# Kernel tuning notes

Measured on AMD Instinct MI355X. Metric: run time of the kernel, lower is better.

The kernel has to match this reference:

```python
import jax, jax.numpy as jnp
import numpy as np

BSZ, SEQ, EMBED = 2, 4096, 1024
NUM_HEADS = 16
HEAD_DIM = EMBED // NUM_HEADS
WINDOW = 256  # attention_window[layer_id]


def setup_inputs() -> dict:
    key = jax.random.key(0)
    ks = jax.random.split(key, 7)
    s = 1.0 / np.sqrt(EMBED)
    return {
        "hidden_states": jax.random.normal(ks[0], (BSZ, SEQ, EMBED), jnp.float32),
        "Wq": jax.random.normal(ks[1], (EMBED, EMBED), jnp.float32) * s,
        "bq": jnp.zeros((EMBED,), jnp.float32),
        "Wk": jax.random.normal(ks[2], (EMBED, EMBED), jnp.float32) * s,
        "bk": jnp.zeros((EMBED,), jnp.float32),
        "Wv": jax.random.normal(ks[3], (EMBED, EMBED), jnp.float32) * s,
        "bv": jnp.zeros((EMBED,), jnp.float32),
    }


def _blocks3(x, nb, w):
    # x: [b, s + 2w, h, d] -> [b, nb, 3w, h, d]; block c sees key blocks c-1, c, c+1
    b = x.shape[0]
    xb = x.reshape(b, nb + 2, w, NUM_HEADS, HEAD_DIM)
    return jnp.concatenate([xb[:, i:i + nb] for i in range(3)], axis=2)


def reference(hidden_states, Wq, bq, Wk, bk, Wv, bv):
    b, s, e = hidden_states.shape
    w = WINDOW
    nb = s // w
    q = (hidden_states @ Wq + bq) * (1.0 / np.sqrt(HEAD_DIM))
    k = hidden_states @ Wk + bk
    v = hidden_states @ Wv + bv
    q = q.reshape(b, nb, w, NUM_HEADS, HEAD_DIM)
    k = k.reshape(b, s, NUM_HEADS, HEAD_DIM)
    v = v.reshape(b, s, NUM_HEADS, HEAD_DIM)
    pad = ((0, 0), (w, w), (0, 0), (0, 0))
    kb = _blocks3(jnp.pad(k, pad), nb, w)  # [b, nb, 3w, h, d]
    vb = _blocks3(jnp.pad(v, pad), nb, w)
    # banded scores: query x in block n attends keys at global pos n*w - w + y
    scores = jnp.einsum('bnxhd,bnyhd->bnhxy', q, kb)  # [b, nb, h, w, 3w]
    x_idx = jnp.arange(w)
    y_idx = jnp.arange(3 * w)
    band = jnp.abs(y_idx[None, :] - x_idx[:, None] - w) <= w  # [w, 3w]
    kpos = jnp.arange(nb)[:, None] * w - w + y_idx[None, :]   # [nb, 3w]
    inb = (kpos >= 0) & (kpos < s)
    mask = band[None, :, :] & inb[:, None, :]                 # [nb, w, 3w]
    scores = jnp.where(mask[None, :, None, :, :], scores, -jnp.inf)
    probs = jax.nn.softmax(scores.astype(jnp.float32), axis=-1).astype(v.dtype)
    attn = jnp.einsum('bnhxy,bnyhd->bnxhd', probs, vb)        # [b, nb, w, h, d]
    return attn.reshape(b, s, e)
```

## Files before the change

kernel.cpp:

```cpp
#include <hip/hip_runtime.h>
#include <stdint.h>

#define SEQ    4096
#define EMBED  1024
#define NHEAD  16
#define HDIM   64
#define WIN    256
#define BSZ    2
#define M_TOT  (BSZ * SEQ)
#define N_QKV  3072
#define N_QK   2048
#define K_DIM  1024
#define LOG2E  1.4426950408889634f

typedef __attribute__((ext_vector_type(8))) __bf16 bf16x8;
typedef __attribute__((ext_vector_type(4))) float  f32x4;

__device__ __forceinline__ unsigned short f2bf(float f) {
  union { float f; unsigned int u; } c; c.f = f;
  unsigned int u = c.u;
  unsigned int r = (u + 0x7FFFu + ((u >> 16) & 1u)) >> 16;
  return (unsigned short)r;
}

__device__ __forceinline__ unsigned int cvt_pk_bf16(float lo, float hi) {
  unsigned int r;
  asm("v_cvt_pk_bf16_f32 %0, %1, %2" : "=v"(r) : "v"(lo), "v"(hi));
  return r;
}

__device__ __forceinline__ void gl2lds16(const void* g, void* l) {
  __builtin_amdgcn_global_load_lds((const __attribute__((address_space(1))) void*)g,
                                   (__attribute__((address_space(3))) void*)l, 16, 0, 0);
}

__global__ __launch_bounds__(256) void cvt_all(const float* __restrict__ in,
                                               unsigned short* __restrict__ out,
                                               const float* __restrict__ Wq,
                                               const float* __restrict__ Wk,
                                               const float* __restrict__ Wv,
                                               unsigned short* __restrict__ Wt) {
  __shared__ float t[32][33];
  int tid = threadIdx.x;
  if (blockIdx.x < 8192) {
    int i = (blockIdx.x * 256 + tid) * 4;
    float4 v = *(const float4*)(in + i);
    ushort4 o;
    o.x = f2bf(v.x); o.y = f2bf(v.y); o.z = f2bf(v.z); o.w = f2bf(v.w);
    *(ushort4*)(out + i) = o;
  } else {
    int wb = blockIdx.x - 8192;
    int z  = wb >> 10;
    int rem = wb & 1023;
    int kb = (rem & 31) * 32, nb = (rem >> 5) * 32;
    const float* W = (z == 0) ? Wq : (z == 1) ? Wk : Wv;
    int tx = tid & 31, ty = tid >> 5;
    for (int it = 0; it < 4; ++it) {
      int k = kb + ty + it * 8;
      t[ty + it * 8][tx] = W[(size_t)k * 1024 + nb + tx];
    }
    __syncthreads();
    for (int it = 0; it < 4; ++it) {
      int n = nb + ty + it * 8;
      Wt[(size_t)(z * 1024 + n) * 1024 + kb + tx] = f2bf(t[tx][ty + it * 8]);
    }
  }
}

__global__ __launch_bounds__(512, 2) void qkv_gemm(const unsigned short* __restrict__ A,
                                                   const unsigned short* __restrict__ Bt,
                                                   const float* __restrict__ bq,
                                                   const float* __restrict__ bk,
                                                   const float* __restrict__ bv,
                                                   unsigned short* __restrict__ C,
                                                   unsigned short* __restrict__ Vt) {
  __shared__ unsigned short As[2][128 * 64];
  __shared__ unsigned short Bs[2][384 * 64];
  int tid  = threadIdx.x;
  int lane = tid & 63, wave = tid >> 6;
  int ln   = lane & 15, quad = lane >> 4;
  int flat = blockIdx.y * 8 + blockIdx.x;
  int swz  = (flat & 7) * 64 + (flat >> 3);
  int m0 = (swz >> 3) * 128, n0 = (swz & 7) * 384;
  int wy = wave >> 2, wx = wave & 3;
  f32x4 acc[4][6];
#pragma unroll
  for (int i = 0; i < 4; ++i)
#pragma unroll
    for (int j = 0; j < 6; ++j) acc[i][j] = (f32x4){0.f, 0.f, 0.f, 0.f};

  int c8 = tid & 7;

#define STG_A(buf, kt)                                                           \
  do {                                                                           \
    _Pragma("unroll")                                                            \
    for (int s = 0; s < 2; ++s) {                                                \
      int r = s * 64 + (tid >> 3); int cg = c8 ^ (r & 7);                        \
      gl2lds16(A + (size_t)(m0 + r) * K_DIM + (size_t)(kt) * 64 + cg * 8,        \
               &As[buf][r * 64 + c8 * 8]);                                       \
    }                                                                            \
  } while (0)
#define STG_B(buf, jreg, kt)                                                     \
  do {                                                                           \
    _Pragma("unroll")                                                            \
    for (int s = 0; s < 2; ++s) {                                                \
      int r = s * 64 + (tid >> 3); int gr = (jreg) * 128 + r;                    \
      int cg = c8 ^ (gr & 7);                                                    \
      gl2lds16(Bt + (size_t)(n0 + gr) * K_DIM + (size_t)(kt) * 64 + cg * 8,      \
               &Bs[buf][gr * 64 + c8 * 8]);                                      \
    }                                                                            \
  } while (0)

  STG_A(0, 0); STG_B(0, 0, 0); STG_B(0, 1, 0); STG_B(0, 2, 0);
  STG_B(1, 0, 1); STG_B(1, 1, 1); STG_B(1, 2, 1);
  asm volatile("s_waitcnt vmcnt(6)" ::: "memory");
  __builtin_amdgcn_s_barrier();

  int aBase = wy * 64, bBase = wx * 96;

#pragma unroll 1
  for (int t = 0; t < 16; ++t) {
    int cur = t & 1;
    const unsigned short* as = As[cur];
    const unsigned short* bs = Bs[cur];
    bf16x8 af[4][2], bf01[2][2], bf23[2][2], bf45[2][2];

#pragma unroll
    for (int i2 = 0; i2 < 4; ++i2) {
      int row = aBase + i2 * 16 + ln;
#pragma unroll
      for (int ks = 0; ks < 2; ++ks) {
        int c = (ks * 4 + quad) ^ (row & 7);
        af[i2][ks] = *(const bf16x8*)&as[row * 64 + c * 8];
      }
    }
#pragma unroll
    for (int j2 = 0; j2 < 2; ++j2) {
      int row = bBase + j2 * 16 + ln;
#pragma unroll
      for (int ks = 0; ks < 2; ++ks) {
        int c = (ks * 4 + quad) ^ (row & 7);
        bf01[j2][ks] = *(const bf16x8*)&bs[row * 64 + c * 8];
      }
    }
    if (t < 15) STG_A(cur ^ 1, t + 1);
    __builtin_amdgcn_s_barrier();
    __builtin_amdgcn_s_setprio(1);
#pragma unroll
    for (int ks = 0; ks < 2; ++ks)
#pragma unroll
      for (int i2 = 0; i2 < 4; ++i2)
#pragma unroll
        for (int j2 = 0; j2 < 2; ++j2)
          acc[i2][j2] = __builtin_amdgcn_mfma_f32_16x16x32_bf16(af[i2][ks], bf01[j2][ks], acc[i2][j2], 0, 0, 0);
    __builtin_amdgcn_s_setprio(0);
    __builtin_amdgcn_s_barrier();

#pragma unroll
    for (int j2 = 0; j2 < 2; ++j2) {
      int row = bBase + 32 + j2 * 16 + ln;
#pragma unroll
      for (int ks = 0; ks < 2; ++ks) {
        int c = (ks * 4 + quad) ^ (row & 7);
        bf23[j2][ks] = *(const bf16x8*)&bs[row * 64 + c * 8];
      }
    }
    __builtin_amdgcn_s_barrier();
    __builtin_amdgcn_s_setprio(1);
#pragma unroll
    for (int ks = 0; ks < 2; ++ks)
#pragma unroll
      for (int i2 = 0; i2 < 4; ++i2)
#pragma unroll
        for (int j2 = 0; j2 < 2; ++j2)
          acc[i2][2 + j2] = __builtin_amdgcn_mfma_f32_16x16x32_bf16(af[i2][ks], bf23[j2][ks], acc[i2][2 + j2], 0, 0, 0);
    __builtin_amdgcn_s_setprio(0);
    __builtin_amdgcn_s_barrier();

#pragma unroll
    for (int j2 = 0; j2 < 2; ++j2) {
      int row = bBase + 64 + j2 * 16 + ln;
#pragma unroll
      for (int ks = 0; ks < 2; ++ks) {
        int c = (ks * 4 + quad) ^ (row & 7);
        bf45[j2][ks] = *(const bf16x8*)&bs[row * 64 + c * 8];
      }
    }
    __builtin_amdgcn_s_barrier();
    __builtin_amdgcn_s_setprio(1);
#pragma unroll
    for (int ks = 0; ks < 2; ++ks)
#pragma unroll
      for (int i2 = 0; i2 < 4; ++i2)
        acc[i2][4] = __builtin_amdgcn_mfma_f32_16x16x32_bf16(af[i2][ks], bf45[0][ks], acc[i2][4], 0, 0, 0);
    __builtin_amdgcn_s_setprio(0);
    if (t < 14) STG_B(cur, 0, t + 2);
    __builtin_amdgcn_s_barrier();

    if (t < 14) { STG_B(cur, 1, t + 2); STG_B(cur, 2, t + 2); }
    __builtin_amdgcn_s_barrier();
    __builtin_amdgcn_s_setprio(1);
#pragma unroll
    for (int ks = 0; ks < 2; ++ks)
#pragma unroll
      for (int i2 = 0; i2 < 4; ++i2)
        acc[i2][5] = __builtin_amdgcn_mfma_f32_16x16x32_bf16(af[i2][ks], bf45[1][ks], acc[i2][5], 0, 0, 0);
    __builtin_amdgcn_s_setprio(0);
    if (t < 14) asm volatile("s_waitcnt vmcnt(6)" ::: "memory");
    else        asm volatile("s_waitcnt vmcnt(0)" ::: "memory");
    __builtin_amdgcn_s_barrier();
  }
#undef STG_A
#undef STG_B

#pragma unroll
  for (int j = 0; j < 6; ++j) {
    int n = n0 + wx * 96 + j * 16 + ln;
    if (n < N_QK) {
      float bias, scl;
      if (n < 1024) { bias = bq[n];        scl = 0.125f * LOG2E; }
      else          { bias = bk[n - 1024]; scl = 1.f; }
#pragma unroll
      for (int i = 0; i < 4; ++i) {
        int mb = m0 + wy * 64 + i * 16 + quad * 4;
#pragma unroll
        for (int r = 0; r < 4; ++r) {
          float v = (acc[i][j][r] + bias) * scl;
          C[(size_t)(mb + r) * N_QK + n] = f2bf(v);
        }
      }
    } else {
      int hd = n - 2048;
      float bias = bv[hd];
#pragma unroll
      for (int i = 0; i < 4; ++i) {
        int mb  = m0 + wy * 64 + i * 16 + quad * 4;
        int bb  = mb >> 12;
        int pos = mb & (SEQ - 1);
        ushort4 pk;
        pk.x = f2bf(acc[i][j][0] + bias);
        pk.y = f2bf(acc[i][j][1] + bias);
        pk.z = f2bf(acc[i][j][2] + bias);
        pk.w = f2bf(acc[i][j][3] + bias);
        *(ushort4*)&Vt[((size_t)bb * (NHEAD * HDIM) + hd) * SEQ + pos] = pk;
      }
    }
  }
}

__global__ __launch_bounds__(256) void attn(const unsigned short* __restrict__ qk,
                                            const unsigned short* __restrict__ vtg,
                                            float* __restrict__ out) {
  __shared__ unsigned short Kl[64 * 72];
  __shared__ unsigned short Vl[64 * 72];
  int tid  = threadIdx.x;
  int lane = tid & 63, wave = tid >> 6;
  int ln   = lane & 15, quad = lane >> 4;
  int bx = blockIdx.x;
  int lx = ((bx & 7) << 3) | (bx >> 3);
  int q0 = lx * 64, head = blockIdx.y, b = blockIdx.z;
  size_t baseRow = (size_t)b * SEQ;
  const unsigned short* kptr = qk + 1024;
  const unsigned short* vrow = vtg + ((size_t)(b * NHEAD + head) * HDIM) * SEQ;

  int sy = tid >> 3, sc = tid & 7;
  const unsigned short* kbase = kptr + (baseRow + sy) * (size_t)N_QK + head * HDIM + sc * 8;
  const unsigned short* vbase = vrow + (size_t)sy * SEQ + sc * 8;

  bf16x8 qf[2];
  {
    size_t ro = (baseRow + q0 + wave * 16 + ln) * (size_t)N_QK + head * HDIM + quad * 8;
    qf[0] = *(const bf16x8*)&qk[ro];
    qf[1] = *(const bf16x8*)&qk[ro + 32];
  }

  float l_st = 0.f;
  f32x4 o_acc[4];
  for (int dt = 0; dt < 4; ++dt) o_acc[dt] = (f32x4){0.f, 0.f, 0.f, 0.f};

  int lo = (q0 >= 256) ? 0 : (256 - q0) / 64;
  int hi = (SEQ + 256 - q0) / 64; if (hi > 9) hi = 9;

  uint4 pkA0, pkA1, pvA0, pvA1;
  uint4 pkB0, pkB1, pvB0, pvB1;
#define PREFETCH_A(KT)                                                      \
  {                                                                         \
    pkA0 = *(const uint4*)&kbase[(size_t)(KT) * N_QK];                      \
    pkA1 = *(const uint4*)&kbase[(size_t)((KT) + 32) * N_QK];               \
    pvA0 = *(const uint4*)&vbase[(KT)];                                     \
    pvA1 = *(const uint4*)&vbase[(size_t)32 * SEQ + (KT)];                  \
  }
#define PREFETCH_B(KT)                                                      \
  {                                                                         \
    pkB0 = *(const uint4*)&kbase[(size_t)(KT) * N_QK];                      \
    pkB1 = *(const uint4*)&kbase[(size_t)((KT) + 32) * N_QK];               \
    pvB0 = *(const uint4*)&vbase[(KT)];                                     \
    pvB1 = *(const uint4*)&vbase[(size_t)32 * SEQ + (KT)];                  \
  }

  PREFETCH_A(q0 - 256 + lo * 64);
  if (lo + 1 < hi) PREFETCH_B(q0 - 256 + (lo + 1) * 64);

  int srcA = ((lane & 16) << 1) | ln;
  int srcB = srcA + 16;
  bool hiQ = (lane & 32) != 0;

  for (int t = lo; t < hi; ++t) {
    int kt = q0 - 256 + t * 64;
    bool useA = ((t - lo) & 1) == 0;

    asm volatile("s_waitcnt lgkmcnt(0)" ::: "memory");
    __builtin_amdgcn_sched_barrier(0);
    __builtin_amdgcn_s_barrier();
    if (useA) {
      *(uint4*)&Kl[sy * 72 + sc * 8]        = pkA0;
      *(uint4*)&Kl[(sy + 32) * 72 + sc * 8] = pkA1;
      *(uint4*)&Vl[sy * 72 + sc * 8]        = pvA0;
      *(uint4*)&Vl[(sy + 32) * 72 + sc * 8] = pvA1;
    } else {
      *(uint4*)&Kl[sy * 72 + sc * 8]        = pkB0;
      *(uint4*)&Kl[(sy + 32) * 72 + sc * 8] = pkB1;
      *(uint4*)&Vl[sy * 72 + sc * 8]        = pvB0;
      *(uint4*)&Vl[(sy + 32) * 72 + sc * 8] = pvB1;
    }
    asm volatile("s_waitcnt lgkmcnt(0)" ::: "memory");
    __builtin_amdgcn_sched_barrier(0);
    __builtin_amdgcn_s_barrier();

    if (t + 2 < hi) {
      if (useA) PREFETCH_A(kt + 128) else PREFETCH_B(kt + 128)
    }

    f32x4 s[4];
    __builtin_amdgcn_s_setprio(1);
    for (int nt = 0; nt < 4; ++nt) {
      bf16x8 kf0 = *(const bf16x8*)&Kl[(nt * 16 + ln) * 72 + quad * 8];
      bf16x8 kf1 = *(const bf16x8*)&Kl[(nt * 16 + ln) * 72 + 32 + quad * 8];
      f32x4 z = (f32x4){0.f, 0.f, 0.f, 0.f};
      z = __builtin_amdgcn_mfma_f32_16x16x32_bf16(kf0, qf[0], z, 0, 0, 0);
      z = __builtin_amdgcn_mfma_f32_16x16x32_bf16(kf1, qf[1], z, 0, 0, 0);
      s[nt] = z;
    }
    __builtin_amdgcn_s_setprio(0);

    if (t == 0 || t == 8) {
      int qq = q0 + wave * 16 + ln;
      for (int nt = 0; nt < 4; ++nt) {
        int kb = kt + nt * 16 + quad * 4 - qq;
        for (int r = 0; r < 4; ++r) {
          int dd = kb + r;
          if (dd < -WIN || dd > WIN) s[nt][r] = -INFINITY;
        }
      }
    }

    float rs = 0.f;
    for (int nt = 0; nt < 4; ++nt)
      for (int r = 0; r < 4; ++r) {
        float p = exp2f(s[nt][r]);
        s[nt][r] = p;
        rs += p;
      }
    l_st += rs;

    unsigned int p01[4], p23[4];
    for (int nt = 0; nt < 4; ++nt) {
      p01[nt] = cvt_pk_bf16(s[nt][0], s[nt][1]);
      p23[nt] = cvt_pk_bf16(s[nt][2], s[nt][3]);
    }

    for (int ks = 0; ks < 2; ++ks) {
      int ntA = 2 * ks, ntB = 2 * ks + 1;
      unsigned int a0 = (unsigned int)__shfl((int)p01[ntA], srcA);
      unsigned int a1 = (unsigned int)__shfl((int)p23[ntA], srcA);
      unsigned int a2 = (unsigned int)__shfl((int)p01[ntA], srcB);
      unsigned int a3 = (unsigned int)__shfl((int)p23[ntA], srcB);
      unsigned int b0 = (unsigned int)__shfl((int)p01[ntB], srcA);
      unsigned int b1 = (unsigned int)__shfl((int)p23[ntB], srcA);
      unsigned int b2 = (unsigned int)__shfl((int)p01[ntB], srcB);
      unsigned int b3 = (unsigned int)__shfl((int)p23[ntB], srcB);
      union { uint4 u; bf16x8 v; } pf;
      pf.u.x = hiQ ? b0 : a0;
      pf.u.y = hiQ ? b1 : a1;
      pf.u.z = hiQ ? b2 : a2;
      pf.u.w = hiQ ? b3 : a3;
      __builtin_amdgcn_s_setprio(1);
      for (int dt = 0; dt < 4; ++dt) {
        bf16x8 vf = *(const bf16x8*)&Vl[(dt * 16 + ln) * 72 + ks * 32 + quad * 8];
        o_acc[dt] = __builtin_amdgcn_mfma_f32_16x16x32_bf16(vf, pf.v, o_acc[dt], 0, 0, 0);
      }
      __builtin_amdgcn_s_setprio(0);
    }
  }

  float l = l_st;
  l += __shfl_xor(l, 16);
  l += __shfl_xor(l, 32);
  float inv = 1.0f / l;
  int qpos = q0 + wave * 16 + ln;
  float* ob = out + (baseRow + qpos) * (size_t)EMBED + head * HDIM + quad * 4;
  for (int dt = 0; dt < 4; ++dt) {
    float4 v;
    v.x = o_acc[dt][0] * inv;
    v.y = o_acc[dt][1] * inv;
    v.z = o_acc[dt][2] * inv;
    v.w = o_acc[dt][3] * inv;
    *(float4*)(ob + dt * 16) = v;
  }
#undef PREFETCH_A
#undef PREFETCH_B
}

extern "C" void kernel_launch(void* const* d_in, const int* in_sizes, int n_in,
                              void* d_out, int out_size, void* d_ws, size_t ws_size,
                              hipStream_t stream) {
  const float* h  = (const float*)d_in[0];
  const float* Wq = (const float*)d_in[1];
  const float* bq = (const float*)d_in[2];
  const float* Wk = (const float*)d_in[3];
  const float* bk = (const float*)d_in[4];
  const float* Wv = (const float*)d_in[5];
  const float* bv = (const float*)d_in[6];
  float* out = (float*)d_out;

  unsigned short* h_bf  = (unsigned short*)d_ws;
  unsigned short* wt_bf = h_bf + (size_t)M_TOT * K_DIM;
  unsigned short* qk    = wt_bf + (size_t)N_QKV * K_DIM;
  unsigned short* vtg   = qk + (size_t)M_TOT * N_QK;

  cvt_all<<<8192 + 3072, 256, 0, stream>>>(h, h_bf, Wq, Wk, Wv, wt_bf);
  qkv_gemm<<<dim3(8, 64), 512, 0, stream>>>(h_bf, wt_bf, bq, bk, bv, qk, vtg);
  attn<<<dim3(SEQ / 64, NHEAD, BSZ), 256, 0, stream>>>(qk, vtg, out);
}
```

Before: 214.5 us.

## Merge GEMM tail MFMA phases and reduce attention prefetch to single buffer

In the QKV GEMM, the B-tile global loads for step t+2 are now issued together before one merged MFMA phase, which drops two barriers per k-step. In the attention kernel, the two-deep register double-buffered K/V prefetch becomes a single-buffer prefetch of the next tile, and the explicit waitcnt/sched_barrier sequences are replaced with __syncthreads. This lowers barrier count and register pressure, but the attention loop gets less prefetch distance to hide global load latency.

After: 207.6 us. 3.2% less time.

```diff
diff --git a/kernel.cpp b/kernel.cpp
--- a/kernel.cpp
+++ b/kernel.cpp
@@ -187,24 +187,15 @@
       }
     }
     __builtin_amdgcn_s_barrier();
+    if (t < 14) { STG_B(cur, 0, t + 2); STG_B(cur, 1, t + 2); STG_B(cur, 2, t + 2); }
     __builtin_amdgcn_s_setprio(1);
 #pragma unroll
     for (int ks = 0; ks < 2; ++ks)
 #pragma unroll
       for (int i2 = 0; i2 < 4; ++i2)
-        acc[i2][4] = __builtin_amdgcn_mfma_f32_16x16x32_bf16(af[i2][ks], bf45[0][ks], acc[i2][4], 0, 0, 0);
-    __builtin_amdgcn_s_setprio(0);
-    if (t < 14) STG_B(cur, 0, t + 2);
-    __builtin_amdgcn_s_barrier();
-
-    if (t < 14) { STG_B(cur, 1, t + 2); STG_B(cur, 2, t + 2); }
-    __builtin_amdgcn_s_barrier();
-    __builtin_amdgcn_s_setprio(1);
-#pragma unroll
-    for (int ks = 0; ks < 2; ++ks)
-#pragma unroll
-      for (int i2 = 0; i2 < 4; ++i2)
-        acc[i2][5] = __builtin_amdgcn_mfma_f32_16x16x32_bf16(af[i2][ks], bf45[1][ks], acc[i2][5], 0, 0, 0);
+#pragma unroll
+        for (int j2 = 0; j2 < 2; ++j2)
+          acc[i2][4 + j2] = __builtin_amdgcn_mfma_f32_16x16x32_bf16(af[i2][ks], bf45[j2][ks], acc[i2][4 + j2], 0, 0, 0);
     __builtin_amdgcn_s_setprio(0);
     if (t < 14) asm volatile("s_waitcnt vmcnt(6)" ::: "memory");
     else        asm volatile("s_waitcnt vmcnt(0)" ::: "memory");
@@ -281,25 +272,16 @@
   int lo = (q0 >= 256) ? 0 : (256 - q0) / 64;
   int hi = (SEQ + 256 - q0) / 64; if (hi > 9) hi = 9;
 
-  uint4 pkA0, pkA1, pvA0, pvA1;
-  uint4 pkB0, pkB1, pvB0, pvB1;
-#define PREFETCH_A(KT)                                                      \
+  uint4 pk0, pk1, pv0, pv1;
+#define PREFETCH(KT)                                                        \
   {                                                                         \
-    pkA0 = *(const uint4*)&kbase[(size_t)(KT) * N_QK];                      \
-    pkA1 = *(const uint4*)&kbase[(size_t)((KT) + 32) * N_QK];               \
-    pvA0 = *(const uint4*)&vbase[(KT)];                                     \
-    pvA1 = *(const uint4*)&vbase[(size_t)32 * SEQ + (KT)];                  \
-  }
-#define PREFETCH_B(KT)                                                      \
-  {                                                                         \
-    pkB0 = *(const uint4*)&kbase[(size_t)(KT) * N_QK];                      \
-    pkB1 = *(const uint4*)&kbase[(size_t)((KT) + 32) * N_QK];               \
-    pvB0 = *(const uint4*)&vbase[(KT)];                                     \
-    pvB1 = *(const uint4*)&vbase[(size_t)32 * SEQ + (KT)];                  \
-  }
-
-  PREFETCH_A(q0 - 256 + lo * 64);
-  if (lo + 1 < hi) PREFETCH_B(q0 - 256 + (lo + 1) * 64);
+    pk0 = *(const uint4*)&kbase[(size_t)(KT) * N_QK];                       \
+    pk1 = *(const uint4*)&kbase[(size_t)((KT) + 32) * N_QK];                \
+    pv0 = *(const uint4*)&vbase[(KT)];                                      \
+    pv1 = *(const uint4*)&vbase[(size_t)32 * SEQ + (KT)];                   \
+  }
+
+  PREFETCH(q0 - 256 + lo * 64);
 
   int srcA = ((lane & 16) << 1) | ln;
   int srcB = srcA + 16;
@@ -307,29 +289,14 @@
 
   for (int t = lo; t < hi; ++t) {
     int kt = q0 - 256 + t * 64;
-    bool useA = ((t - lo) & 1) == 0;
-
-    asm volatile("s_waitcnt lgkmcnt(0)" ::: "memory");
-    __builtin_amdgcn_sched_barrier(0);
-    __builtin_amdgcn_s_barrier();
-    if (useA) {
-      *(uint4*)&Kl[sy * 72 + sc * 8]        = pkA0;
-      *(uint4*)&Kl[(sy + 32) * 72 + sc * 8] = pkA1;
-      *(uint4*)&Vl[sy * 72 + sc * 8]        = pvA0;
-      *(uint4*)&Vl[(sy + 32) * 72 + sc * 8] = pvA1;
-    } else {
-      *(uint4*)&Kl[sy * 72 + sc * 8]        = pkB0;
-      *(uint4*)&Kl[(sy + 32) * 72 + sc * 8] = pkB1;
-      *(uint4*)&Vl[sy * 72 + sc * 8]        = pvB0;
-      *(uint4*)&Vl[(sy + 32) * 72 + sc * 8] = pvB1;
-    }
-    asm volatile("s_waitcnt lgkmcnt(0)" ::: "memory");
-    __builtin_amdgcn_sched_barrier(0);
-    __builtin_amdgcn_s_barrier();
-
-    if (t + 2 < hi) {
-      if (useA) PREFETCH_A(kt + 128) else PREFETCH_B(kt + 128)
-    }
+    __syncthreads();
+    *(uint4*)&Kl[sy * 72 + sc * 8]        = pk0;
+    *(uint4*)&Kl[(sy + 32) * 72 + sc * 8] = pk1;
+    *(uint4*)&Vl[sy * 72 + sc * 8]        = pv0;
+    *(uint4*)&Vl[(sy + 32) * 72 + sc * 8] = pv1;
+    __syncthreads();
+
+    if (t + 1 < hi) { PREFETCH(kt + 64); }
 
     f32x4 s[4];
     __builtin_amdgcn_s_setprio(1);
@@ -407,8 +374,7 @@
     v.w = o_acc[dt][3] * inv;
     *(float4*)(ob + dt * 16) = v;
   }
-#undef PREFETCH_A
-#undef PREFETCH_B
+#undef PREFETCH
 }
 
 extern "C" void kernel_launch(void* const* d_in, const int* in_sizes, int n_in,
```
